# Kernel optimization log

Hardware: AMD Instinct MI355X
Metric: run time of the kernel (lower is better)

## Reference

```python
import jax, jax.numpy as jnp
import numpy as np

TEMPERATURE = 0.07
BASE_TEMPERATURE = 0.07


def setup_inputs() -> dict:
    key = jax.random.key(0)
    k1, k2 = jax.random.split(key)
    N, D = 8192, 512
    features = jax.random.normal(k1, (N, D), dtype=jnp.float32)
    labels = jax.random.randint(k2, (N,), 0, 64, dtype=jnp.int64 if jax.config.jax_enable_x64 else jnp.int32)
    return {"features": features, "labels": labels, "rotation_multiplier": 2}


def reference(features, labels, rotation_multiplier):
    k = int(rotation_multiplier)
    N = features.shape[0]
    B = N // k
    # L2-normalize rows (torch F.normalize clamps norm at eps=1e-12)
    norm = jnp.maximum(jnp.linalg.norm(features, axis=1, keepdims=True), 1e-12)
    f = features / norm
    sim = jnp.matmul(f, f.T) / TEMPERATURE  # [N, N]

    # block positive mask: groups of k rows share a label; compare group labels
    lab = labels.reshape(B, k)[:, 0]  # [B]
    same = lab[:, None] == lab[None, :]  # [B, B]
    mask = jnp.repeat(jnp.repeat(same, k, axis=0), k, axis=1)  # [N, N]
    eye = jnp.eye(N, dtype=bool)
    mask = mask & ~eye

    # stable masked log-softmax with diagonal removed from denominator
    logits_max = jax.lax.stop_gradient(jnp.max(sim, axis=1, keepdims=True))
    logits = sim - logits_max
    exp_logits = jnp.exp(logits)
    denom = exp_logits.sum(axis=1, keepdims=True) - jnp.diagonal(exp_logits)[:, None] + 1e-8
    log_prob = logits - jnp.log(denom)

    mask_f = mask.astype(logits.dtype)
    mask_sum = mask_f.sum(axis=1)  # [N]
    valid = mask_sum > 0
    mean_log_prob_pos = (log_prob * mask_f).sum(axis=1) / jnp.maximum(mask_sum, 1.0)
    per_sample = -(TEMPERATURE / BASE_TEMPERATURE) * mean_log_prob_pos
    n_valid = valid.sum().astype(logits.dtype)
    loss = jnp.where(valid, per_sample, 0.0).sum() / jnp.maximum(n_valid, 1.0)
    return loss
```

## Files before the change

### kernel.cpp

```cpp
#include <hip/hip_runtime.h>
#include <hip/hip_bf16.h>

#define TEMP_INV 14.285714285714286f
#define FSCALE 16.0f
#define T1S (TEMP_INV / 256.0f)
#define INV_LN2 1.4426950408889634f
#define LN2F 0.6931471805599453f
#define T1S2 (T1S * INV_LN2)
#define TI2  (TEMP_INV * INV_LN2)

typedef __attribute__((ext_vector_type(4))) float f32x4;
typedef __attribute__((ext_vector_type(4))) int i32x4;
typedef __attribute__((ext_vector_type(8))) int i32x8;


__global__ __launch_bounds__(256) void norm_k(const float* __restrict__ feat,
                                              uchar* __restrict__ fq,
                                              const int* __restrict__ labels,
                                              const int* __restrict__ kptr,
                                              int* __restrict__ glab,
                                              float* __restrict__ gacc,
                                              int* __restrict__ dcnt,
                                              int N, int D) {
  const int row = (blockIdx.x * 256 + threadIdx.x) >> 6;
  const int lane = threadIdx.x & 63;
  if (row < N) {
    const float4* fr = (const float4*)(feat + (size_t)row * D);
    float4 v0 = fr[lane * 2];
    float4 v1 = fr[lane * 2 + 1];
    float ss = v0.x * v0.x + v0.y * v0.y + v0.z * v0.z + v0.w * v0.w +
               v1.x * v1.x + v1.y * v1.y + v1.z * v1.z + v1.w * v1.w;
    #pragma unroll
    for (int off = 32; off; off >>= 1) ss += __shfl_xor(ss, off, 64);
    const float inv = FSCALE / fmaxf(sqrtf(ss), 1e-12f);
    int w0 = 0, w1 = 0;
    w0 = __builtin_amdgcn_cvt_pk_fp8_f32(v0.x * inv, v0.y * inv, w0, false);
    w0 = __builtin_amdgcn_cvt_pk_fp8_f32(v0.z * inv, v0.w * inv, w0, true);
    w1 = __builtin_amdgcn_cvt_pk_fp8_f32(v1.x * inv, v1.y * inv, w1, false);
    w1 = __builtin_amdgcn_cvt_pk_fp8_f32(v1.z * inv, v1.w * inv, w1, true);
    uint2 o; o.x = (uint)w0; o.y = (uint)w1;
    const int tkb  = lane >> 4;
    const int quad = (lane >> 2) & 3;
    const int half = (lane >> 1) & 1;
    const int slot = half * 64 + quad * 16 + (row & 15);
    uchar* dstp = fq + (((size_t)(row >> 4) * (D >> 7) + tkb) << 11) +
                  slot * 16 + (lane & 1) * 8;
    *(uint2*)dstp = o;
    if (lane == 0) {
      const int k = *kptr;
      glab[row] = labels[(size_t)(row / k) * k];
    }
  }
  if (blockIdx.x == 0 && threadIdx.x < 3) {
    if (threadIdx.x < 2) gacc[threadIdx.x] = 0.f;
    else *dcnt = 0;
  }
}

__global__ __launch_bounds__(128) void gemm_k(const uchar* __restrict__ fq,
                                              const int* __restrict__ glab,
                                              float* __restrict__ partS,
                                              float* __restrict__ partP,
                                              int N, int D) {
  const int lane = threadIdx.x & 63;
  const int wid  = threadIdx.x >> 6;
  const int quad = lane >> 4, l15 = lane & 15;
  const int ktiles = D >> 7;
  const int strip = (blockIdx.x >> 3) * 2 + wid;
  const int slice = blockIdx.x & 7;
  const int r0 = strip * 32;
  const int cps = N >> 3;
  const int jsteps = cps >> 6;
  const int j0base = slice * cps;

  int diagJ = -1;
  if (r0 >= j0base && r0 < j0base + cps) diagJ = (r0 - j0base) >> 6;

  int rlab[2][4];
  #pragma unroll
  for (int mi = 0; mi < 2; mi++)
    #pragma unroll
    for (int r = 0; r < 4; r++)
      rlab[mi][r] = glab[r0 + mi * 16 + quad * 4 + r];

  float Srun[2][4] = {{0.f, 0.f, 0.f, 0.f}, {0.f, 0.f, 0.f, 0.f}};
  float Prun[2][4] = {{0.f, 0.f, 0.f, 0.f}, {0.f, 0.f, 0.f, 0.f}};

#define LOADF(dst, grp, kt)                                                   \
  {                                                                           \
    const uchar* p_ = fq + (((size_t)((grp) * ktiles + (kt))) << 11) + lane * 16; \
    i32x4 lo_ = *(const i32x4*)p_;                                            \
    i32x4 hi_ = *(const i32x4*)(p_ + 1024);                                   \
    dst = (i32x8){lo_.x, lo_.y, lo_.z, lo_.w, hi_.x, hi_.y, hi_.z, hi_.w};    \
  }

#define EPILOG_FAST(j0)                                                       \
  {                                                                           \
    int clab[4];                                                              \
    _Pragma("unroll")                                                         \
    for (int ni = 0; ni < 4; ni++) clab[ni] = glab[(j0) + ni * 16 + l15];     \
    _Pragma("unroll")                                                         \
    for (int mi = 0; mi < 2; mi++)                                            \
      _Pragma("unroll")                                                       \
      for (int r = 0; r < 4; r++) {                                           \
        const int rl = rlab[mi][r];                                           \
        float s = 0.f, pp = 0.f;                                              \
        _Pragma("unroll")                                                     \
        for (int ni = 0; ni < 4; ni++) {                                      \
          const float lg2 = fmaf(acc[mi][ni][r], T1S2, -TI2);                 \
          s += exp2f(lg2);                                                    \
          pp += (rl == clab[ni]) ? lg2 : 0.f;                                 \
        }                                                                     \
        Srun[mi][r] += s;                                                     \
        Prun[mi][r] += pp;                                                    \
      }                                                                       \
  }

#define EPILOG_DIAG(j0)                                                       \
  {                                                                           \
    int clab[4];                                                              \
    _Pragma("unroll")                                                         \
    for (int ni = 0; ni < 4; ni++) clab[ni] = glab[(j0) + ni * 16 + l15];     \
    _Pragma("unroll")                                                         \
    for (int mi = 0; mi < 2; mi++)                                            \
      _Pragma("unroll")                                                       \
      for (int r = 0; r < 4; r++) {                                           \
        const int row = r0 + mi * 16 + quad * 4 + r;                          \
        const int rl = rlab[mi][r];                                           \
        float s = 0.f, pp = 0.f;                                              \
        _Pragma("unroll")                                                     \
        for (int ni = 0; ni < 4; ni++) {                                      \
          const int col = (j0) + ni * 16 + l15;                               \
          const float lg2 = fmaf(acc[mi][ni][r], T1S2, -TI2);                 \
          const bool diag = (col == row);                                     \
          s += diag ? 0.f : exp2f(lg2);                                       \
          pp += (!diag && rl == clab[ni]) ? lg2 : 0.f;                        \
        }                                                                     \
        Srun[mi][r] += s;                                                     \
        Prun[mi][r] += pp;                                                    \
      }                                                                       \
  }

  if (ktiles == 4) {
    i32x8 af[2][4];
    #pragma unroll
    for (int mi = 0; mi < 2; mi++)
      #pragma unroll
      for (int kt = 0; kt < 4; kt++)
        LOADF(af[mi][kt], (r0 >> 4) + mi, kt)

    for (int js = 0; js < jsteps; js++) {
      const int j0 = j0base + js * 64;
      f32x4 acc[2][4];
      #pragma unroll
      for (int mi = 0; mi < 2; mi++)
        #pragma unroll
        for (int ni = 0; ni < 4; ni++) {
          f32x4 z = {0.f, 0.f, 0.f, 0.f};
          acc[mi][ni] = z;
        }
      #pragma unroll
      for (int kt = 0; kt < 4; kt++) {
        i32x8 bv[4];
        #pragma unroll
        for (int ni = 0; ni < 4; ni++)
          LOADF(bv[ni], (j0 >> 4) + ni, kt)
        #pragma unroll
        for (int mi = 0; mi < 2; mi++)
          #pragma unroll
          for (int ni = 0; ni < 4; ni++)
            acc[mi][ni] = __builtin_amdgcn_mfma_scale_f32_16x16x128_f8f6f4(
                af[mi][kt], bv[ni], acc[mi][ni], 0, 0, 0, 127, 0, 127);
      }
      if (js == diagJ) { EPILOG_DIAG(j0) } else { EPILOG_FAST(j0) }
    }
  } else {
    for (int js = 0; js < jsteps; js++) {
      const int j0 = j0base + js * 64;
      f32x4 acc[2][4];
      #pragma unroll
      for (int mi = 0; mi < 2; mi++)
        #pragma unroll
        for (int ni = 0; ni < 4; ni++) {
          f32x4 z = {0.f, 0.f, 0.f, 0.f};
          acc[mi][ni] = z;
        }
      for (int kt = 0; kt < ktiles; kt++) {
        i32x8 as[2], bv[4];
        #pragma unroll
        for (int mi = 0; mi < 2; mi++) LOADF(as[mi], (r0 >> 4) + mi, kt)
        #pragma unroll
        for (int ni = 0; ni < 4; ni++) LOADF(bv[ni], (j0 >> 4) + ni, kt)
        #pragma unroll
        for (int mi = 0; mi < 2; mi++)
          #pragma unroll
          for (int ni = 0; ni < 4; ni++)
            acc[mi][ni] = __builtin_amdgcn_mfma_scale_f32_16x16x128_f8f6f4(
                as[mi], bv[ni], acc[mi][ni], 0, 0, 0, 127, 0, 127);
      }
      if (js == diagJ) { EPILOG_DIAG(j0) } else { EPILOG_FAST(j0) }
    }
  }
#undef LOADF
#undef EPILOG_FAST
#undef EPILOG_DIAG

  #pragma unroll
  for (int mi = 0; mi < 2; mi++)
    #pragma unroll
    for (int r = 0; r < 4; r++) {
      float s = Srun[mi][r], p = Prun[mi][r];
      #pragma unroll
      for (int off = 1; off < 16; off <<= 1) {
        s += __shfl_xor(s, off, 64);
        p += __shfl_xor(p, off, 64);
      }
      if (l15 == 0) {
        const int row = r0 + mi * 16 + quad * 4 + r;
        partS[(size_t)row * 8 + slice] = s;
        partP[(size_t)row * 8 + slice] = p * LN2F;
      }
    }
}

__global__ __launch_bounds__(256) void reduce_loss_k(const float* __restrict__ partS,
                                                     const float* __restrict__ partP,
                                                     const int* __restrict__ glab,
                                                     const int* __restrict__ labels,
                                                     const int* __restrict__ kptr,
                                                     float* __restrict__ gacc,
                                                     int* __restrict__ dcnt,
                                                     float* __restrict__ out, int N) {
  const int tt = threadIdx.x;
  const int row = blockIdx.x * 256 + tt;
  const int k = *kptr;
  const int B = N / k;

  __shared__ int h[64];
  if (tt < 64) h[tt] = 0;
  __syncthreads();
  for (int g = tt; g < B; g += 256) {
    int lb = labels[(size_t)g * k];
    if (lb >= 0 && lb < 64) atomicAdd(&h[lb], 1);
  }
  __syncthreads();

  float l = 0.f, v = 0.f;
  if (row < N) {
    float S = 0.f, P = 0.f;
    #pragma unroll
    for (int s = 0; s < 8; s++) {
      S += partS[(size_t)row * 8 + s];
      P += partP[(size_t)row * 8 + s];
    }
    const int np = h[glab[row]] * k - 1;
    if (np > 0) {
      l = -(P - (float)np * logf(S + 1e-8f)) / (float)np;
      v = 1.f;
    }
  }
  #pragma unroll
  for (int off = 32; off; off >>= 1) {
    l += __shfl_xor(l, off, 64);
    v += __shfl_xor(v, off, 64);
  }
  __shared__ float sl4[4], sv4[4];
  if ((tt & 63) == 0) { sl4[tt >> 6] = l; sv4[tt >> 6] = v; }
  __syncthreads();
  if (tt == 0) {
    float L = 0.f, V = 0.f;
    #pragma unroll
    for (int i = 0; i < 4; i++) { L += sl4[i]; V += sv4[i]; }
    atomicAdd(&gacc[0], L);
    atomicAdd(&gacc[1], V);
    __threadfence();
    const int prev = atomicAdd(dcnt, 1);
    if (prev == (int)gridDim.x - 1) {
      const float Lf = atomicAdd(&gacc[0], 0.f);
      const float Vf = atomicAdd(&gacc[1], 0.f);
      out[0] = Lf / fmaxf(Vf, 1.f);
    }
  }
}

extern "C" void kernel_launch(void* const* d_in, const int* in_sizes, int n_in,
                              void* d_out, int out_size, void* d_ws, size_t ws_size,
                              hipStream_t stream) {
  const float* feat = (const float*)d_in[0];
  const int* labels = (const int*)d_in[1];
  const int* kptr   = (const int*)d_in[2];
  const int N = in_sizes[1];
  const int D = in_sizes[0] / N;

  char* ws = (char*)d_ws;
  uchar* fq = (uchar*)ws;
  size_t off = (size_t)N * D;
  float* partS = (float*)(ws + off); off += (size_t)N * 8 * sizeof(float);
  float* partP = (float*)(ws + off); off += (size_t)N * 8 * sizeof(float);
  int* glab    = (int*)(ws + off);   off += (size_t)N * sizeof(int);
  float* gacc  = (float*)(ws + off); off += 2 * sizeof(float);
  int* dcnt    = (int*)(ws + off);   off += sizeof(int);

  const int strips = N / 32;
  const int ggrid = (strips / 2) * 8;

  norm_k<<<(N + 3) / 4, 256, 0, stream>>>(feat, fq, labels, kptr, glab,
                                          gacc, dcnt, N, D);
  gemm_k<<<ggrid, 128, 0, stream>>>(fq, glab, partS, partP, N, D);
  reduce_loss_k<<<(N + 255) / 256, 256, 0, stream>>>(partS, partP, glab, labels,
                                                     kptr, gacc, dcnt,
                                                     (float*)d_out, N);
}
```

Before: 127.4 us.

## Exploit similarity symmetry: compute upper-triangle tiles and scatter column sums via atomics

The GEMM now computes only the upper triangle of the symmetric similarity matrix. Each 32x32 tile's exp-sums and positive-logit sums feed both the row accumulators and, through atomicAdd, the column accumulators colS/colP. Work is balanced by pairing strip p with strip nstrips-1-p inside each block. Tiles shrink from 32x64 to 32x32, cutting the MFMA work and exp count roughly in half, at the cost of global atomics, more cross-lane shuffles and smaller tiles with less B reuse.

```diff
diff --git a/kernel.cpp b/kernel.cpp
--- a/kernel.cpp
+++ b/kernel.cpp
@@ -8,6 +8,7 @@
 #define LN2F 0.6931471805599453f
 #define T1S2 (T1S * INV_LN2)
 #define TI2  (TEMP_INV * INV_LN2)
+#define NS 8
 
 typedef __attribute__((ext_vector_type(4))) float f32x4;
 typedef __attribute__((ext_vector_type(4))) int i32x4;
@@ -19,11 +20,15 @@
                                               const int* __restrict__ labels,
                                               const int* __restrict__ kptr,
                                               int* __restrict__ glab,
+                                              float* __restrict__ colS,
+                                              float* __restrict__ colP,
                                               float* __restrict__ gacc,
                                               int* __restrict__ dcnt,
                                               int N, int D) {
   const int row = (blockIdx.x * 256 + threadIdx.x) >> 6;
   const int lane = threadIdx.x & 63;
+  const int gtid = blockIdx.x * 256 + threadIdx.x;
+  if (gtid < N) { colS[gtid] = 0.f; colP[gtid] = 0.f; }
   if (row < N) {
     const float4* fr = (const float4*)(feat + (size_t)row * D);
     float4 v0 = fr[lane * 2];
@@ -61,20 +66,18 @@
                                               const int* __restrict__ glab,
                                               float* __restrict__ partS,
                                               float* __restrict__ partP,
+                                              float* __restrict__ colS,
+                                              float* __restrict__ colP,
                                               int N, int D) {
   const int lane = threadIdx.x & 63;
   const int wid  = threadIdx.x >> 6;
   const int quad = lane >> 4, l15 = lane & 15;
   const int ktiles = D >> 7;
-  const int strip = (blockIdx.x >> 3) * 2 + wid;
-  const int slice = blockIdx.x & 7;
-  const int r0 = strip * 32;
-  const int cps = N >> 3;
-  const int jsteps = cps >> 6;
-  const int j0base = slice * cps;
-
-  int diagJ = -1;
-  if (r0 >= j0base && r0 < j0base + cps) diagJ = (r0 - j0base) >> 6;
+  const int nstrips = N >> 5;
+  const int p = (int)(blockIdx.x / NS);
+  const int s = (int)(blockIdx.x % NS);
+  const int a = wid ? (nstrips - 1 - p) : p;
+  const int r0 = a << 5;
 
   int rlab[2][4];
   #pragma unroll
@@ -89,55 +92,62 @@
 #define LOADF(dst, grp, kt)                                                   \
   {                                                                           \
     const uchar* p_ = fq + (((size_t)((grp) * ktiles + (kt))) << 11) + lane * 16; \
-    i32x4 lo_ = *(const i32x4*)p_;                                            \
-    i32x4 hi_ = *(const i32x4*)(p_ + 1024);                                   \
-    dst = (i32x8){lo_.x, lo_.y, lo_.z, lo_.w, hi_.x, hi_.y, hi_.z, hi_.w};    \
-  }
-
-#define EPILOG_FAST(j0)                                                       \
+    i32x4* d_ = (i32x4*)&(dst);                                               \
+    d_[0] = *(const i32x4*)p_;                                                \
+    d_[1] = *(const i32x4*)(p_ + 1024);                                       \
+  }
+
+#define EPILOG_FAST(c0)                                                       \
   {                                                                           \
-    int clab[4];                                                              \
-    _Pragma("unroll")                                                         \
-    for (int ni = 0; ni < 4; ni++) clab[ni] = glab[(j0) + ni * 16 + l15];     \
+    int clab[2];                                                              \
+    clab[0] = glab[(c0) + l15];                                               \
+    clab[1] = glab[(c0) + 16 + l15];                                          \
+    float colE[2] = {0.f, 0.f}, colQ[2] = {0.f, 0.f};                         \
     _Pragma("unroll")                                                         \
     for (int mi = 0; mi < 2; mi++)                                            \
       _Pragma("unroll")                                                       \
       for (int r = 0; r < 4; r++) {                                           \
         const int rl = rlab[mi][r];                                           \
-        float s = 0.f, pp = 0.f;                                              \
         _Pragma("unroll")                                                     \
-        for (int ni = 0; ni < 4; ni++) {                                      \
+        for (int ni = 0; ni < 2; ni++) {                                      \
           const float lg2 = fmaf(acc[mi][ni][r], T1S2, -TI2);                 \
-          s += exp2f(lg2);                                                    \
-          pp += (rl == clab[ni]) ? lg2 : 0.f;                                 \
+          const float e = exp2f(lg2);                                         \
+          const float pm = (rl == clab[ni]) ? lg2 : 0.f;                      \
+          Srun[mi][r] += e; Prun[mi][r] += pm;                                \
+          colE[ni] += e; colQ[ni] += pm;                                      \
         }                                                                     \
-        Srun[mi][r] += s;                                                     \
-        Prun[mi][r] += pp;                                                    \
       }                                                                       \
-  }
-
-#define EPILOG_DIAG(j0)                                                       \
+    _Pragma("unroll")                                                         \
+    for (int ni = 0; ni < 2; ni++) {                                          \
+      float e = colE[ni], q = colQ[ni];                                       \
+      e += __shfl_xor(e, 16, 64); e += __shfl_xor(e, 32, 64);                 \
+      q += __shfl_xor(q, 16, 64); q += __shfl_xor(q, 32, 64);                 \
+      if (quad == 0) {                                                        \
+        atomicAdd(&colS[(c0) + ni * 16 + l15], e);                            \
+        atomicAdd(&colP[(c0) + ni * 16 + l15], q * LN2F);                     \
+      }                                                                       \
+    }                                                                         \
+  }
+
+#define EPILOG_DIAG(c0)                                                       \
   {                                                                           \
-    int clab[4];                                                              \
-    _Pragma("unroll")                                                         \
-    for (int ni = 0; ni < 4; ni++) clab[ni] = glab[(j0) + ni * 16 + l15];     \
+    int clab[2];                                                              \
+    clab[0] = glab[(c0) + l15];                                               \
+    clab[1] = glab[(c0) + 16 + l15];                                          \
     _Pragma("unroll")                                                         \
     for (int mi = 0; mi < 2; mi++)                                            \
       _Pragma("unroll")                                                       \
       for (int r = 0; r < 4; r++) {                                           \
         const int row = r0 + mi * 16 + quad * 4 + r;                          \
         const int rl = rlab[mi][r];                                           \
-        float s = 0.f, pp = 0.f;                                              \
         _Pragma("unroll")                                                     \
-        for (int ni = 0; ni < 4; ni++) {                                      \
-          const int col = (j0) + ni * 16 + l15;                               \
+        for (int ni = 0; ni < 2; ni++) {                                      \
+          const int col = (c0) + ni * 16 + l15;                               \
           const float lg2 = fmaf(acc[mi][ni][r], T1S2, -TI2);                 \
           const bool diag = (col == row);                                     \
-          s += diag ? 0.f : exp2f(lg2);                                       \
-          pp += (!diag && rl == clab[ni]) ? lg2 : 0.f;                        \
+          Srun[mi][r] += diag ? 0.f : exp2f(lg2);                             \
+          Prun[mi][r] += (!diag && rl == clab[ni]) ? lg2 : 0.f;               \
         }                                                                     \
-        Srun[mi][r] += s;                                                     \
-        Prun[mi][r] += pp;                                                    \
       }                                                                       \
   }
 
@@ -149,56 +159,57 @@
       for (int kt = 0; kt < 4; kt++)
         LOADF(af[mi][kt], (r0 >> 4) + mi, kt)
 
-    for (int js = 0; js < jsteps; js++) {
-      const int j0 = j0base + js * 64;
-      f32x4 acc[2][4];
+    for (int jb = a + s; jb < nstrips; jb += NS) {
+      const int c0 = jb << 5;
+      f32x4 acc[2][2];
       #pragma unroll
       for (int mi = 0; mi < 2; mi++)
         #pragma unroll
-        for (int ni = 0; ni < 4; ni++) {
+        for (int ni = 0; ni < 2; ni++) {
           f32x4 z = {0.f, 0.f, 0.f, 0.f};
           acc[mi][ni] = z;
         }
-      #pragma unroll
-      for (int kt = 0; kt < 4; kt++) {
-        i32x8 bv[4];
+      i32x8 bv[2][4];
+      #pragma unroll
+      for (int ni = 0; ni < 2; ni++)
         #pragma unroll
-        for (int ni = 0; ni < 4; ni++)
-          LOADF(bv[ni], (j0 >> 4) + ni, kt)
+        for (int kt = 0; kt < 4; kt++)
+          LOADF(bv[ni][kt], (c0 >> 4) + ni, kt)
+      #pragma unroll
+      for (int kt = 0; kt < 4; kt++)
         #pragma unroll
         for (int mi = 0; mi < 2; mi++)
           #pragma unroll
-          for (int ni = 0; ni < 4; ni++)
+          for (int ni = 0; ni < 2; ni++)
             acc[mi][ni] = __builtin_amdgcn_mfma_scale_f32_16x16x128_f8f6f4(
-                af[mi][kt], bv[ni], acc[mi][ni], 0, 0, 0, 127, 0, 127);
-      }
-      if (js == diagJ) { EPILOG_DIAG(j0) } else { EPILOG_FAST(j0) }
+                af[mi][kt], bv[ni][kt], acc[mi][ni], 0, 0, 0, 127, 0, 127);
+      if (jb == a) { EPILOG_DIAG(c0) } else { EPILOG_FAST(c0) }
     }
   } else {
-    for (int js = 0; js < jsteps; js++) {
-      const int j0 = j0base + js * 64;
-      f32x4 acc[2][4];
+    for (int jb = a + s; jb < nstrips; jb += NS) {
+      const int c0 = jb << 5;
+      f32x4 acc[2][2];
       #pragma unroll
       for (int mi = 0; mi < 2; mi++)
         #pragma unroll
-        for (int ni = 0; ni < 4; ni++) {
+        for (int ni = 0; ni < 2; ni++) {
           f32x4 z = {0.f, 0.f, 0.f, 0.f};
           acc[mi][ni] = z;
         }
       for (int kt = 0; kt < ktiles; kt++) {
-        i32x8 as[2], bv[4];
-        #pragma unroll
-        for (int mi = 0; mi < 2; mi++) LOADF(as[mi], (r0 >> 4) + mi, kt)
-        #pragma unroll
-        for (int ni = 0; ni < 4; ni++) LOADF(bv[ni], (j0 >> 4) + ni, kt)
-        #pragma unroll
-        for (int mi = 0; mi < 2; mi++)
-          #pragma unroll
-          for (int ni = 0; ni < 4; ni++)
-            acc[mi][ni] = __builtin_amdgcn_mfma_scale_f32_16x16x128_f8f6f4(
-                as[mi], bv[ni], acc[mi][ni], 0, 0, 0, 127, 0, 127);
+        i32x8 a0, a1, b0, b1;
+        LOADF(a0, (r0 >> 4) + 0, kt) LOADF(a1, (r0 >> 4) + 1, kt)
+        LOADF(b0, (c0 >> 4) + 0, kt) LOADF(b1, (c0 >> 4) + 1, kt)
+        acc[0][0] = __builtin_amdgcn_mfma_scale_f32_16x16x128_f8f6f4(
+            a0, b0, acc[0][0], 0, 0, 0, 127, 0, 127);
+        acc[0][1] = __builtin_amdgcn_mfma_scale_f32_16x16x128_f8f6f4(
+            a0, b1, acc[0][1], 0, 0, 0, 127, 0, 127);
+        acc[1][0] = __builtin_amdgcn_mfma_scale_f32_16x16x128_f8f6f4(
+            a1, b0, acc[1][0], 0, 0, 0, 127, 0, 127);
+        acc[1][1] = __builtin_amdgcn_mfma_scale_f32_16x16x128_f8f6f4(
+            a1, b1, acc[1][1], 0, 0, 0, 127, 0, 127);
       }
-      if (js == diagJ) { EPILOG_DIAG(j0) } else { EPILOG_FAST(j0) }
+      if (jb == a) { EPILOG_DIAG(c0) } else { EPILOG_FAST(c0) }
     }
   }
 #undef LOADF
@@ -209,22 +220,24 @@
   for (int mi = 0; mi < 2; mi++)
     #pragma unroll
     for (int r = 0; r < 4; r++) {
-      float s = Srun[mi][r], p = Prun[mi][r];
+      float sv = Srun[mi][r], pv = Prun[mi][r];
       #pragma unroll
       for (int off = 1; off < 16; off <<= 1) {
-        s += __shfl_xor(s, off, 64);
-        p += __shfl_xor(p, off, 64);
+        sv += __shfl_xor(sv, off, 64);
+        pv += __shfl_xor(pv, off, 64);
       }
       if (l15 == 0) {
         const int row = r0 + mi * 16 + quad * 4 + r;
-        partS[(size_t)row * 8 + slice] = s;
-        partP[(size_t)row * 8 + slice] = p * LN2F;
+        partS[(size_t)row * NS + s] = sv;
+        partP[(size_t)row * NS + s] = pv * LN2F;
       }
     }
 }
 
 __global__ __launch_bounds__(256) void reduce_loss_k(const float* __restrict__ partS,
                                                      const float* __restrict__ partP,
+                                                     const float* __restrict__ colS,
+                                                     const float* __restrict__ colP,
                                                      const int* __restrict__ glab,
                                                      const int* __restrict__ labels,
                                                      const int* __restrict__ kptr,
@@ -247,11 +260,11 @@
 
   float l = 0.f, v = 0.f;
   if (row < N) {
-    float S = 0.f, P = 0.f;
-    #pragma unroll
-    for (int s = 0; s < 8; s++) {
-      S += partS[(size_t)row * 8 + s];
-      P += partP[(size_t)row * 8 + s];
+    float S = colS[row], P = colP[row];
+    #pragma unroll
+    for (int s = 0; s < NS; s++) {
+      S += partS[(size_t)row * NS + s];
+      P += partP[(size_t)row * NS + s];
     }
     const int np = h[glab[row]] * k - 1;
     if (np > 0) {
@@ -295,19 +308,21 @@
   char* ws = (char*)d_ws;
   uchar* fq = (uchar*)ws;
   size_t off = (size_t)N * D;
-  float* partS = (float*)(ws + off); off += (size_t)N * 8 * sizeof(float);
-  float* partP = (float*)(ws + off); off += (size_t)N * 8 * sizeof(float);
+  float* partS = (float*)(ws + off); off += (size_t)N * NS * sizeof(float);
+  float* partP = (float*)(ws + off); off += (size_t)N * NS * sizeof(float);
+  float* colS  = (float*)(ws + off); off += (size_t)N * sizeof(float);
+  float* colP  = (float*)(ws + off); off += (size_t)N * sizeof(float);
   int* glab    = (int*)(ws + off);   off += (size_t)N * sizeof(int);
   float* gacc  = (float*)(ws + off); off += 2 * sizeof(float);
   int* dcnt    = (int*)(ws + off);   off += sizeof(int);
 
-  const int strips = N / 32;
-  const int ggrid = (strips / 2) * 8;
+  const int nstrips = N / 32;
+  const int ggrid = (nstrips / 2) * NS;
 
   norm_k<<<(N + 3) / 4, 256, 0, stream>>>(feat, fq, labels, kptr, glab,
-                                          gacc, dcnt, N, D);
-  gemm_k<<<ggrid, 128, 0, stream>>>(fq, glab, partS, partP, N, D);
-  reduce_loss_k<<<(N + 255) / 256, 256, 0, stream>>>(partS, partP, glab, labels,
-                                                     kptr, gacc, dcnt,
-                                                     (float*)d_out, N);
+                                          colS, colP, gacc, dcnt, N, D);
+  gemm_k<<<ggrid, 128, 0, stream>>>(fq, glab, partS, partP, colS, colP, N, D);
+  reduce_loss_k<<<(N + 255) / 256, 256, 0, stream>>>(partS, partP, colS, colP,
+                                                     glab, labels, kptr, gacc,
+                                                     dcnt, (float*)d_out, N);
 }
```

New measurement: 155.1 us. 21.7% more time.
